# Optimization experiments

Hardware: AMD Instinct MI355X
Metric: run time of the kernel (lower is better)

## Reference

```python
import jax, jax.numpy as jnp
import numpy as np

N = 50000   # nodes
E = 800000  # edges (avg degree 16)
IN = 128    # in_dim
R = 4       # rank
CMB = 64    # combine_dim
H = 4       # heads
D = 64      # hidden_dim per head
NEG_SLOPE = 0.2


def setup_inputs() -> dict:
    key = jax.random.key(0)
    ks = iter(jax.random.split(key, 24))
    def rnd(shape, s):
        return jax.random.normal(next(ks), shape, jnp.float32) * s
    src = jax.random.randint(next(ks), (E,), 0, N, jnp.int32)
    dst = jax.random.randint(next(ks), (E,), 0, N, jnp.int32)
    ones = jnp.ones((N, 1), jnp.float32)
    # buffers built in __init__: features with a trailing ones column
    h_common = jnp.concatenate([rnd((N, IN), 1.0), ones], axis=-1)      # (N, 129)
    h_type = jnp.concatenate([rnd((N, 512), 1.0), ones], axis=-1)       # (N, 513)
    h_rel = jnp.concatenate([rnd((N, 512), 1.0), ones], axis=-1)        # (N, 513)
    return {
        'src': src, 'dst': dst,
        'h_common': h_common, 'h_type': h_type, 'h_rel': h_rel,
        'Wc': rnd((R, IN + 1, CMB), 0.05),
        'Wt': rnd((R, 513, CMB), 0.05),
        'Wr': rnd((R, 513, CMB), 0.05),
        'fw': rnd((1, R), 0.5),
        'fb': rnd((1, CMB), 0.1),
        'W0': rnd((CMB, H * D), 0.05),
        'al0': rnd((H, D), 0.05), 'ar0': rnd((H, D), 0.05),
        'b0': rnd((H * D,), 0.05),
        'W1': rnd((H * D, H * D), 0.05),
        'al1': rnd((H, D), 0.05), 'ar1': rnd((H, D), 0.05),
        'b1': rnd((H * D,), 0.05),
    }


def _gat_layer(h, src, dst, W, al, ar, b, residual):
    # h: (N, F_in) -> out: (N, H*D), attention a: (E, H)
    feat = (h @ W).reshape(N, H, D)
    el = jnp.einsum('nhd,hd->nh', feat, al)  # (N, H)
    er = jnp.einsum('nhd,hd->nh', feat, ar)
    e = jax.nn.leaky_relu(el[src] + er[dst], NEG_SLOPE)  # (E, H)
    # edge softmax over incoming edges of each dst node
    m = jax.ops.segment_max(e, dst, num_segments=N)      # (N, H)
    ee = jnp.exp(e - m[dst])
    s = jax.ops.segment_sum(ee, dst, num_segments=N)
    a = ee / s[dst]                                       # (E, H)
    msg = feat[src] * a[:, :, None]                       # (E, H, D)
    out = jax.ops.segment_sum(msg, dst, num_segments=N)   # (N, H, D)
    if residual:
        out = out + h.reshape(N, H, D)
    out = out + b.reshape(1, H, D)
    return out.reshape(N, H * D), a


def reference(src, dst, h_common, h_type, h_rel, Wc, Wt, Wr, fw, fb,
              W0, al0, ar0, b0, W1, al1, ar1, b1):
    # low-rank trilinear fusion
    fc = jnp.einsum('ni,ric->rnc', h_common, Wc)  # (R, N, CMB)
    ft = jnp.einsum('ni,ric->rnc', h_type, Wt)
    fr = jnp.einsum('ni,ric->rnc', h_rel, Wr)
    zy = fc * ft * fr
    h = jnp.einsum('r,rnc->nc', fw[0], zy) + fb   # (N, CMB)
    h = jax.nn.elu(h)
    # stacked GAT layers
    h, att = _gat_layer(h, src, dst, W0, al0, ar0, b0, residual=False)
    h, att = _gat_layer(h, src, dst, W1, al1, ar1, b1, residual=True)
    return h, att
```

## Files before the change

kernel.cpp:

```cpp
#include <hip/hip_runtime.h>
#include <math.h>

#define NN 50000
#define EE 800000
#define NEG 0.2f
#define NG (NN / 16)

using f32x4  = __attribute__((ext_vector_type(4))) float;
using bf16x8 = __attribute__((ext_vector_type(8))) short;

__device__ __forceinline__ float lrelu(float x){ return x > 0.f ? x : NEG*x; }

__device__ __forceinline__ unsigned short f2b(float f){
    unsigned int u = __float_as_uint(f);
    return (unsigned short)((u + 0x7FFFu + ((u >> 16) & 1u)) >> 16);
}
__device__ __forceinline__ float b2f(unsigned short h){
    return __uint_as_float(((unsigned int)h) << 16);
}

__global__ void pack_w_fusion(const float* __restrict__ W, unsigned short* __restrict__ out,
                              int K, int NKC)
{
    int u = blockIdx.x * blockDim.x + threadIdx.x;
    if (u >= NKC * 16 * 64) return;
    int l = u & 63, chunk = (u >> 6) & 15, kc = u >> 10;
    int ct = chunk >> 2, r = chunk & 3;
    int c = ct * 16 + (l & 15);
    int kb = kc * 32 + (l >> 4) * 8;
    bf16x8 v;
#pragma unroll
    for (int j = 0; j < 8; ++j)
        v[j] = (short)f2b(W[((size_t)r * K + kb + j) * 64 + c]);
    *(bf16x8*)(out + (size_t)u * 8) = v;
}

template<int PERM>
__global__ void pack_w_gemm(const float* __restrict__ W, unsigned short* __restrict__ out,
                            int K, int C)
{
    int NCH = C / 16;
    int total = (K / 32) * NCH * 64;
    int u = blockIdx.x * blockDim.x + threadIdx.x;
    if (u >= total) return;
    int l = u & 63, ch = (u >> 6) % NCH, kc = u / (64 * NCH);
    int c = ch * 16 + (l & 15);
    int kb = kc * 32 + (l >> 4) * 8;
    bf16x8 v;
#pragma unroll
    for (int j = 0; j < 8; ++j) {
        int k = kb + j;
        int ko = PERM ? ((k & 3) * 64 + (k >> 2)) : k;
        v[j] = (short)f2b(W[(size_t)ko * C + c]);
    }
    *(bf16x8*)(out + (size_t)u * 8) = v;
}

template<int KT, int NKC>
__global__ __launch_bounds__(256) void pack_a_tile(
    const float* __restrict__ F, unsigned short* __restrict__ out)
{
    constexpr int TILES = NKC / 4;
    __shared__ float sf[16][130];
    const int tid = threadIdx.x;
    const int g = blockIdx.x / TILES, t = blockIdx.x % TILES;
    const int nb = g * 16, k0 = t * 128;

#pragma unroll
    for (int i = 0; i < 8; ++i) {
        int idx = tid + i * 256;
        int row = idx >> 7, k = idx & 127;
        sf[row][k] = F[(size_t)(nb + row) * KT + k0 + k];
    }
    __syncthreads();
    {
        int kcl = tid >> 6, l = tid & 63;
        int row = l & 15, kb = kcl * 32 + (l >> 4) * 8;
        bf16x8 o;
#pragma unroll
        for (int j = 0; j < 8; ++j) o[j] = (short)f2b(sf[row][kb + j]);
        *(bf16x8*)(out + ((size_t)(g * NKC + t * 4 + kcl) * 64 + l) * 8) = o;
    }
}

template<int K, int NKC>
__device__ __forceinline__ void fusion_pass_rank(
    const unsigned short* __restrict__ ap, const unsigned short* __restrict__ wp,
    const float* __restrict__ W, int G, int w, int l, f32x4 (&acc)[4])
{
    const int c_lo = l & 15;
#pragma unroll
    for (int ct = 0; ct < 4; ++ct) {
        float wi = W[((size_t)w * K + (K - 1)) * 64 + ct * 16 + c_lo];
        acc[ct] = f32x4{wi, wi, wi, wi};
    }
    const unsigned short* ab = ap + (size_t)G * NKC * 512 + l * 8;
    constexpr int D = (NKC < 8) ? NKC : 8;
#pragma unroll
    for (int h = 0; h < NKC / D; ++h) {
        bf16x8 afs[D];
#pragma unroll
        for (int j = 0; j < D; ++j)
            afs[j] = *(const bf16x8*)(ab + (h * D + j) * 512);
        bf16x8 bcur[4];
        {
            const unsigned short* wk = wp + (size_t)(h * D) * 8192 + w * 512 + l * 8;
#pragma unroll
            for (int i = 0; i < 4; ++i) bcur[i] = *(const bf16x8*)(wk + i * 2048);
        }
#pragma unroll
        for (int j = 0; j < D; ++j) {
            bf16x8 bnxt[4];
            if (j + 1 < D) {
                const unsigned short* wk = wp + (size_t)(h * D + j + 1) * 8192 + w * 512 + l * 8;
#pragma unroll
                for (int i = 0; i < 4; ++i) bnxt[i] = *(const bf16x8*)(wk + i * 2048);
            }
#pragma unroll
            for (int i = 0; i < 4; ++i)
                acc[i] = __builtin_amdgcn_mfma_f32_16x16x32_bf16(afs[j], bcur[i], acc[i], 0, 0, 0);
            if (j + 1 < D) {
#pragma unroll
                for (int i = 0; i < 4; ++i) bcur[i] = bnxt[i];
            }
        }
    }
}

__global__ __launch_bounds__(256) void fusion_mfma(
    const unsigned short* __restrict__ apc, const unsigned short* __restrict__ apt,
    const unsigned short* __restrict__ apr,
    const unsigned short* __restrict__ wpc, const unsigned short* __restrict__ wpt,
    const unsigned short* __restrict__ wpr,
    const float* __restrict__ Wc, const float* __restrict__ Wt, const float* __restrict__ Wr,
    const float* __restrict__ fw, const float* __restrict__ fb,
    unsigned short* __restrict__ h0b)
{
    __shared__ float lds[4096];
    const int w = threadIdx.x >> 6, l = threadIdx.x & 63;
    const int G = blockIdx.x;

    f32x4 prod[4], acc[4];
    fusion_pass_rank<129, 4>(apc, wpc, Wc, G, w, l, acc);
#pragma unroll
    for (int ct = 0; ct < 4; ++ct) prod[ct] = acc[ct];
    fusion_pass_rank<513, 16>(apt, wpt, Wt, G, w, l, acc);
#pragma unroll
    for (int ct = 0; ct < 4; ++ct) prod[ct] *= acc[ct];
    fusion_pass_rank<513, 16>(apr, wpr, Wr, G, w, l, acc);
    const float fww = fw[w];
#pragma unroll
    for (int ct = 0; ct < 4; ++ct) {
        prod[ct] = prod[ct] * acc[ct] * fww;
        *(f32x4*)&lds[((w * 4 + ct) * 64 + l) * 4] = prod[ct];
    }
    __syncthreads();

    f32x4 s = *(const f32x4*)&lds[((0 * 4 + w) * 64 + l) * 4];
#pragma unroll
    for (int r = 1; r < 4; ++r)
        s += *(const f32x4*)&lds[((r * 4 + w) * 64 + l) * 4];

    const int c = w * 16 + (l & 15);
    const float fbc = fb[c];
#pragma unroll
    for (int q = 0; q < 4; ++q) {
        int n = G * 16 + (l >> 4) * 4 + q;
        float v = s[q] + fbc;
        v = v > 0.f ? v : expm1f(v);
        h0b[(size_t)n * 64 + c] = f2b(v);
    }
}

template<int K>
__global__ __launch_bounds__(256) void gemm_reg(
    const unsigned short* __restrict__ Ab, const unsigned short* __restrict__ wp,
    unsigned short* __restrict__ featb)
{
    constexpr int NKC = K / 32;
    const int w = threadIdx.x >> 6, l = threadIdx.x & 63;
    const int nb = blockIdx.x * 16;

    f32x4 acc[4];
#pragma unroll
    for (int i = 0; i < 4; ++i) acc[i] = f32x4{0.f, 0.f, 0.f, 0.f};

    const unsigned short* abase = Ab + (size_t)(nb + (l & 15)) * K + (l >> 4) * 8;
    bf16x8 afs[NKC];
#pragma unroll
    for (int kc = 0; kc < NKC; ++kc)
        afs[kc] = *(const bf16x8*)(abase + kc * 32);

    bf16x8 bcur[4];
    {
        const unsigned short* wk = wp + (size_t)(0 * 16 + w * 4) * 512 + l * 8;
#pragma unroll
        for (int i = 0; i < 4; ++i) bcur[i] = *(const bf16x8*)(wk + i * 512);
    }
#pragma unroll
    for (int kc = 0; kc < NKC; ++kc) {
        bf16x8 bnxt[4];
        if (kc + 1 < NKC) {
            const unsigned short* wk = wp + ((size_t)(kc + 1) * 16 + w * 4) * 512 + l * 8;
#pragma unroll
            for (int i = 0; i < 4; ++i) bnxt[i] = *(const bf16x8*)(wk + i * 512);
        }
#pragma unroll
        for (int i = 0; i < 4; ++i)
            acc[i] = __builtin_amdgcn_mfma_f32_16x16x32_bf16(afs[kc], bcur[i], acc[i], 0, 0, 0);
        if (kc + 1 < NKC) {
#pragma unroll
            for (int i = 0; i < 4; ++i) bcur[i] = bnxt[i];
        }
    }
#pragma unroll
    for (int i = 0; i < 4; ++i) {
        int c = (w * 4 + i) * 16 + (l & 15);
        int dm = (c & 63) * 4 + (c >> 6);
#pragma unroll
        for (int q = 0; q < 4; ++q) {
            int n = nb + (l >> 4) * 4 + q;
            featb[(size_t)n * 256 + dm] = f2b(acc[i][q]);
        }
    }
}

__global__ __launch_bounds__(256) void elr_kernel(
    const unsigned short* __restrict__ featb,
    const float* __restrict__ al, const float* __restrict__ ar,
    float* __restrict__ el, float* __restrict__ er)
{
    int wid = (int)((blockIdx.x * (size_t)blockDim.x + threadIdx.x) >> 6);
    int lane = threadIdx.x & 63;
    if (wid >= NN) return;
    ushort4 f4 = *(const ushort4*)(featb + (size_t)wid * 256 + lane * 4);
    float x0 = b2f(f4.x), x1 = b2f(f4.y), x2 = b2f(f4.z), x3 = b2f(f4.w);
    float elh[4], erh[4];
    elh[0] = x0 * al[lane];        erh[0] = x0 * ar[lane];
    elh[1] = x1 * al[64 + lane];   erh[1] = x1 * ar[64 + lane];
    elh[2] = x2 * al[128 + lane];  erh[2] = x2 * ar[128 + lane];
    elh[3] = x3 * al[192 + lane];  erh[3] = x3 * ar[192 + lane];
#pragma unroll
    for (int off = 32; off; off >>= 1) {
#pragma unroll
        for (int h = 0; h < 4; ++h) {
            elh[h] += __shfl_xor(elh[h], off);
            erh[h] += __shfl_xor(erh[h], off);
        }
    }
    if (lane == 0) {
        *(float4*)(el + (size_t)wid * 4) = make_float4(elh[0], elh[1], elh[2], elh[3]);
        *(float4*)(er + (size_t)wid * 4) = make_float4(erh[0], erh[1], erh[2], erh[3]);
    }
}

__global__ void hist_kernel(const int* __restrict__ dst, int* __restrict__ cnt)
{
    int e = blockIdx.x * blockDim.x + threadIdx.x;
    if (e < EE) atomicAdd(&cnt[dst[e]], 1);
}

__global__ __launch_bounds__(1024) void scan_kernel(const int* __restrict__ cnt, int* __restrict__ offs)
{
    __shared__ int tmp[1024];
    const int t = threadIdx.x;
    const int C = (NN + 1023) / 1024;
    int lo = t * C, hi = min(lo + C, NN);
    int s = 0;
    for (int i = lo; i < hi; ++i) s += cnt[i];
    tmp[t] = s;
    __syncthreads();
    for (int off = 1; off < 1024; off <<= 1) {
        int v = (t >= off) ? tmp[t - off] : 0;
        __syncthreads();
        tmp[t] += v;
        __syncthreads();
    }
    int run = (t == 0) ? 0 : tmp[t - 1];
    for (int i = lo; i < hi; ++i) { offs[i] = run; run += cnt[i]; }
    if (t == 1023) offs[NN] = tmp[1023];
}

__global__ void scatter_kernel(const int* __restrict__ dst, const int* __restrict__ offs,
                               int* __restrict__ cur, int* __restrict__ esort)
{
    int e = blockIdx.x * blockDim.x + threadIdx.x;
    if (e < EE) {
        int d = dst[e];
        int p = offs[d] + atomicAdd(&cur[d], 1);
        esort[p] = e;
    }
}

__global__ void edge_prep(const int* __restrict__ esort, const int* __restrict__ src,
                          const int* __restrict__ dst,
                          const float* __restrict__ el, const float* __restrict__ er,
                          float4* __restrict__ eesort, int* __restrict__ srcsort)
{
    int p = blockIdx.x * blockDim.x + threadIdx.x;
    if (p >= EE) return;
    int e = esort[p];
    int s = src[e], d = dst[e];
    srcsort[p] = s;
    float4 l4 = *(const float4*)(el + (size_t)s * 4);
    float4 r4 = *(const float4*)(er + (size_t)d * 4);
    eesort[p] = make_float4(lrelu(l4.x + r4.x), lrelu(l4.y + r4.y),
                            lrelu(l4.z + r4.z), lrelu(l4.w + r4.w));
}

template <int RESID, int WMZ, int WB16, int WF32>
__global__ __launch_bounds__(256) void gat_agg(
    const int* __restrict__ srcsort, const int* __restrict__ offs,
    const unsigned short* __restrict__ featb, float4* __restrict__ eesort,
    const unsigned short* __restrict__ residb, const float* __restrict__ bias,
    float* __restrict__ out, unsigned short* __restrict__ outb,
    float4* __restrict__ mbuf, float4* __restrict__ zbuf)
{
    int n = (int)((blockIdx.x * (size_t)blockDim.x + threadIdx.x) >> 6);
    int lane = threadIdx.x & 63;
    if (n >= NN) return;
    int s0 = offs[n], s1 = offs[n + 1];

    float m0 = -1e30f, m1 = -1e30f, m2 = -1e30f, m3 = -1e30f;
    for (int p = s0 + lane; p < s1; p += 64) {
        float4 v = eesort[p];
        m0 = fmaxf(m0, v.x); m1 = fmaxf(m1, v.y);
        m2 = fmaxf(m2, v.z); m3 = fmaxf(m3, v.w);
    }
#pragma unroll
    for (int off = 32; off; off >>= 1) {
        m0 = fmaxf(m0, __shfl_xor(m0, off));
        m1 = fmaxf(m1, __shfl_xor(m1, off));
        m2 = fmaxf(m2, __shfl_xor(m2, off));
        m3 = fmaxf(m3, __shfl_xor(m3, off));
    }

    float z0 = 0.f, z1 = 0.f, z2 = 0.f, z3 = 0.f;
    for (int p = s0 + lane; p < s1; p += 64) {
        float4 v = eesort[p];
        v.x = expf(v.x - m0); v.y = expf(v.y - m1);
        v.z = expf(v.z - m2); v.w = expf(v.w - m3);
        eesort[p] = v;
        z0 += v.x; z1 += v.y; z2 += v.z; z3 += v.w;
    }
    __threadfence_block();
#pragma unroll
    for (int off = 32; off; off >>= 1) {
        z0 += __shfl_xor(z0, off);
        z1 += __shfl_xor(z1, off);
        z2 += __shfl_xor(z2, off);
        z3 += __shfl_xor(z3, off);
    }
    float i0 = z0 > 0.f ? 1.f / z0 : 0.f;
    float i1 = z1 > 0.f ? 1.f / z1 : 0.f;
    float i2 = z2 > 0.f ? 1.f / z2 : 0.f;
    float i3 = z3 > 0.f ? 1.f / z3 : 0.f;
    if (WMZ && lane == 0) {
        mbuf[n] = make_float4(m0, m1, m2, m3);
        zbuf[n] = make_float4(i0, i1, i2, i3);
    }

    float a0 = 0.f, a1 = 0.f, a2 = 0.f, a3 = 0.f;
    float c0 = 0.f, c1 = 0.f, c2 = 0.f, c3 = 0.f;
    int p = s0;
    for (; p + 3 < s1; p += 4) {
        float4 wA = eesort[p],     wB = eesort[p + 1];
        float4 wC = eesort[p + 2], wD = eesort[p + 3];
        int sA = srcsort[p],     sB = srcsort[p + 1];
        int sC = srcsort[p + 2], sD = srcsort[p + 3];
        ushort4 fA = *(const ushort4*)(featb + (size_t)sA * 256 + lane * 4);
        ushort4 fB = *(const ushort4*)(featb + (size_t)sB * 256 + lane * 4);
        ushort4 fC = *(const ushort4*)(featb + (size_t)sC * 256 + lane * 4);
        ushort4 fD = *(const ushort4*)(featb + (size_t)sD * 256 + lane * 4);
        a0 += wA.x * b2f(fA.x);  c0 += wB.x * b2f(fB.x);
        a1 += wA.y * b2f(fA.y);  c1 += wB.y * b2f(fB.y);
        a2 += wA.z * b2f(fA.z);  c2 += wB.z * b2f(fB.z);
        a3 += wA.w * b2f(fA.w);  c3 += wB.w * b2f(fB.w);
        a0 += wC.x * b2f(fC.x);  c0 += wD.x * b2f(fD.x);
        a1 += wC.y * b2f(fC.y);  c1 += wD.y * b2f(fD.y);
        a2 += wC.z * b2f(fC.z);  c2 += wD.z * b2f(fD.z);
        a3 += wC.w * b2f(fC.w);  c3 += wD.w * b2f(fD.w);
    }
    for (; p < s1; ++p) {
        float4 wA = eesort[p];
        int sA = srcsort[p];
        ushort4 fA = *(const ushort4*)(featb + (size_t)sA * 256 + lane * 4);
        a0 += wA.x * b2f(fA.x);
        a1 += wA.y * b2f(fA.y);
        a2 += wA.z * b2f(fA.z);
        a3 += wA.w * b2f(fA.w);
    }
    a0 += c0; a1 += c1; a2 += c2; a3 += c3;

    float o0 = a0 * i0 + bias[lane];
    float o1 = a1 * i1 + bias[64 + lane];
    float o2 = a2 * i2 + bias[128 + lane];
    float o3 = a3 * i3 + bias[192 + lane];
    if (RESID) {
        ushort4 rp = *(const ushort4*)(residb + (size_t)n * 256 + lane * 4);
        o0 += b2f(rp.x); o1 += b2f(rp.y); o2 += b2f(rp.z); o3 += b2f(rp.w);
    }
    if (WF32) {
        float* op = out + (size_t)n * 256;
        op[lane] = o0;
        op[64 + lane] = o1;
        op[128 + lane] = o2;
        op[192 + lane] = o3;
    }
    if (WB16) {
        ushort4 ob;
        ob.x = f2b(o0); ob.y = f2b(o1); ob.z = f2b(o2); ob.w = f2b(o3);
        *(ushort4*)(outb + (size_t)n * 256 + lane * 4) = ob;
    }
}

__global__ void att_final(const int* __restrict__ src, const int* __restrict__ dst,
                          const float* __restrict__ el, const float* __restrict__ er,
                          const float4* __restrict__ mbuf, const float4* __restrict__ zbuf,
                          float4* __restrict__ att)
{
    int e = blockIdx.x * blockDim.x + threadIdx.x;
    if (e >= EE) return;
    int s = src[e], d = dst[e];
    float4 l4 = *(const float4*)(el + (size_t)s * 4);
    float4 r4 = *(const float4*)(er + (size_t)d * 4);
    float4 m4 = mbuf[d], zi = zbuf[d];
    att[e] = make_float4(expf(lrelu(l4.x + r4.x) - m4.x) * zi.x,
                         expf(lrelu(l4.y + r4.y) - m4.y) * zi.y,
                         expf(lrelu(l4.z + r4.z) - m4.z) * zi.z,
                         expf(lrelu(l4.w + r4.w) - m4.w) * zi.w);
}

extern "C" void kernel_launch(void* const* d_in, const int* in_sizes, int n_in,
                              void* d_out, int out_size, void* d_ws, size_t ws_size,
                              hipStream_t stream)
{
    const int*   src = (const int*)d_in[0];
    const int*   dst = (const int*)d_in[1];
    const float* hc  = (const float*)d_in[2];
    const float* ht  = (const float*)d_in[3];
    const float* hr  = (const float*)d_in[4];
    const float* Wc  = (const float*)d_in[5];
    const float* Wt  = (const float*)d_in[6];
    const float* Wr  = (const float*)d_in[7];
    const float* fw  = (const float*)d_in[8];
    const float* fb  = (const float*)d_in[9];
    const float* W0  = (const float*)d_in[10];
    const float* al0 = (const float*)d_in[11];
    const float* ar0 = (const float*)d_in[12];
    const float* b0  = (const float*)d_in[13];
    const float* W1  = (const float*)d_in[14];
    const float* al1 = (const float*)d_in[15];
    const float* ar1 = (const float*)d_in[16];
    const float* b1  = (const float*)d_in[17];

    char* ws = (char*)d_ws;
    unsigned short* h0b   = (unsigned short*)(ws);
    unsigned short* h1b   = (unsigned short*)(ws + 6400000);
    unsigned short* featb = (unsigned short*)(ws + 32000000);
    float* el    = (float*)(ws + 57600000);
    float* er    = (float*)(ws + 58400000);
    int*   cnt   = (int*)  (ws + 59200000);
    int*   offs  = (int*)  (ws + 59400000);
    int*   esort = (int*)  (ws + 59600128);
    unsigned short* wpc = (unsigned short*)(ws + 62800128);
    unsigned short* wpt = (unsigned short*)(ws + 62865664);
    unsigned short* wpr = (unsigned short*)(ws + 63127808);
    unsigned short* wp0 = (unsigned short*)(ws + 63389952);
    unsigned short* wp1 = (unsigned short*)(ws + 63422720);
    float4* mbuf = (float4*)(ws + 63553792);
    float4* zbuf = (float4*)(ws + 64353792);
    int* srcsort = (int*)  (ws + 65153792);
    if (ws_size < 68353792ull) return;

    float* outh = (float*)d_out;
    float4* atto = (float4*)(outh + (size_t)NN * 256);

    unsigned short* apt = (unsigned short*)d_out;
    unsigned short* apc = (unsigned short*)((char*)d_out + 51200000);
    unsigned short* apr = (unsigned short*)(ws + 6400000);

    pack_w_fusion<<<(4 * 16 * 64 + 255) / 256, 256, 0, stream>>>(Wc, wpc, 129, 4);
    pack_w_fusion<<<(16 * 16 * 64 + 255) / 256, 256, 0, stream>>>(Wt, wpt, 513, 16);
    pack_w_fusion<<<(16 * 16 * 64 + 255) / 256, 256, 0, stream>>>(Wr, wpr, 513, 16);
    pack_w_gemm<0><<<(2 * 16 * 64 + 255) / 256, 256, 0, stream>>>(W0, wp0, 64, 256);
    pack_w_gemm<1><<<(8 * 16 * 64 + 255) / 256, 256, 0, stream>>>(W1, wp1, 256, 256);

    pack_a_tile<129, 4><<<NG * 1, 256, 0, stream>>>(hc, apc);
    pack_a_tile<513, 16><<<NG * 4, 256, 0, stream>>>(ht, apt);
    pack_a_tile<513, 16><<<NG * 4, 256, 0, stream>>>(hr, apr);

    fusion_mfma<<<NG, 256, 0, stream>>>(apc, apt, apr, wpc, wpt, wpr,
                                        Wc, Wt, Wr, fw, fb, h0b);

    hipMemsetAsync(cnt, 0, NN * sizeof(int), stream);
    hist_kernel<<<(EE + 255) / 256, 256, 0, stream>>>(dst, cnt);
    scan_kernel<<<1, 1024, 0, stream>>>(cnt, offs);
    hipMemsetAsync(cnt, 0, NN * sizeof(int), stream);
    scatter_kernel<<<(EE + 255) / 256, 256, 0, stream>>>(dst, offs, cnt, esort);

    gemm_reg<64><<<NG, 256, 0, stream>>>(h0b, wp0, featb);
    elr_kernel<<<(NN * 64 + 255) / 256, 256, 0, stream>>>(featb, al0, ar0, el, er);
    edge_prep<<<(EE + 255) / 256, 256, 0, stream>>>(esort, src, dst, el, er, atto, srcsort);
    gat_agg<0, 0, 1, 0><<<(NN * 64 + 255) / 256, 256, 0, stream>>>(
        srcsort, offs, featb, atto, nullptr, b0, nullptr, h1b, nullptr, nullptr);

    gemm_reg<256><<<NG, 256, 0, stream>>>(h1b, wp1, featb);
    elr_kernel<<<(NN * 64 + 255) / 256, 256, 0, stream>>>(featb, al1, ar1, el, er);
    edge_prep<<<(EE + 255) / 256, 256, 0, stream>>>(esort, src, dst, el, er, atto, srcsort);
    gat_agg<1, 1, 0, 1><<<(NN * 64 + 255) / 256, 256, 0, stream>>>(
        srcsort, offs, featb, atto, h1b, b1, outh, nullptr, mbuf, zbuf);
    att_final<<<(EE + 255) / 256, 256, 0, stream>>>(src, dst, el, er, mbuf, zbuf, atto);
}
```

Before: 628.8 us.

## Split fusion GEMM K-dimension across two wave groups with LDS reduction

The fusion kernel now runs 512 threads per block. Each rank is handled by two waves that each process half of the K chunks for the common, type and relation projections, and the partial sums are combined through LDS before the trilinear product and the rank reduction. This doubles the waves per 16-row tile to expose more memory-level parallelism and shorten the per-wave serial MFMA chain. In exchange it adds several block barriers, twice the LDS, and drops the explicit software prefetch of weight fragments.

Measured after the change: 637.4 us. Within noise of the previous version (+1.4%).

```diff
diff --git a/kernel.cpp b/kernel.cpp
--- a/kernel.cpp
+++ b/kernel.cpp
@@ -84,50 +84,36 @@
 }
 
 template<int K, int NKC>
-__device__ __forceinline__ void fusion_pass_rank(
+__device__ __forceinline__ void fusion_pass_half(
     const unsigned short* __restrict__ ap, const unsigned short* __restrict__ wp,
-    const float* __restrict__ W, int G, int w, int l, f32x4 (&acc)[4])
-{
+    const float* __restrict__ W, int G, int r, int kh, int l, f32x4 (&acc)[4])
+{
+    constexpr int H = NKC / 2;
     const int c_lo = l & 15;
 #pragma unroll
     for (int ct = 0; ct < 4; ++ct) {
-        float wi = W[((size_t)w * K + (K - 1)) * 64 + ct * 16 + c_lo];
-        acc[ct] = f32x4{wi, wi, wi, wi};
-    }
-    const unsigned short* ab = ap + (size_t)G * NKC * 512 + l * 8;
-    constexpr int D = (NKC < 8) ? NKC : 8;
-#pragma unroll
-    for (int h = 0; h < NKC / D; ++h) {
-        bf16x8 afs[D];
-#pragma unroll
-        for (int j = 0; j < D; ++j)
-            afs[j] = *(const bf16x8*)(ab + (h * D + j) * 512);
-        bf16x8 bcur[4];
-        {
-            const unsigned short* wk = wp + (size_t)(h * D) * 8192 + w * 512 + l * 8;
-#pragma unroll
-            for (int i = 0; i < 4; ++i) bcur[i] = *(const bf16x8*)(wk + i * 2048);
-        }
-#pragma unroll
-        for (int j = 0; j < D; ++j) {
-            bf16x8 bnxt[4];
-            if (j + 1 < D) {
-                const unsigned short* wk = wp + (size_t)(h * D + j + 1) * 8192 + w * 512 + l * 8;
-#pragma unroll
-                for (int i = 0; i < 4; ++i) bnxt[i] = *(const bf16x8*)(wk + i * 2048);
-            }
-#pragma unroll
-            for (int i = 0; i < 4; ++i)
-                acc[i] = __builtin_amdgcn_mfma_f32_16x16x32_bf16(afs[j], bcur[i], acc[i], 0, 0, 0);
-            if (j + 1 < D) {
-#pragma unroll
-                for (int i = 0; i < 4; ++i) bcur[i] = bnxt[i];
-            }
-        }
-    }
-}
-
-__global__ __launch_bounds__(256) void fusion_mfma(
+        if (kh == 0) {
+            float wi = W[((size_t)r * K + (K - 1)) * 64 + ct * 16 + c_lo];
+            acc[ct] = f32x4{wi, wi, wi, wi};
+        } else {
+            acc[ct] = f32x4{0.f, 0.f, 0.f, 0.f};
+        }
+    }
+    const unsigned short* ab = ap + (size_t)G * NKC * 512 + (size_t)kh * H * 512 + l * 8;
+    const unsigned short* wb = wp + (size_t)kh * H * 8192 + r * 512 + l * 8;
+#pragma unroll
+    for (int kc = 0; kc < H; ++kc) {
+        bf16x8 af = *(const bf16x8*)(ab + kc * 512);
+        const unsigned short* wk = wb + (size_t)kc * 8192;
+#pragma unroll
+        for (int ct = 0; ct < 4; ++ct) {
+            bf16x8 bf = *(const bf16x8*)(wk + ct * 2048);
+            acc[ct] = __builtin_amdgcn_mfma_f32_16x16x32_bf16(af, bf, acc[ct], 0, 0, 0);
+        }
+    }
+}
+
+__global__ __launch_bounds__(512) void fusion_mfma(
     const unsigned short* __restrict__ apc, const unsigned short* __restrict__ apt,
     const unsigned short* __restrict__ apr,
     const unsigned short* __restrict__ wpc, const unsigned short* __restrict__ wpt,
@@ -136,39 +122,69 @@
     const float* __restrict__ fw, const float* __restrict__ fb,
     unsigned short* __restrict__ h0b)
 {
-    __shared__ float lds[4096];
-    const int w = threadIdx.x >> 6, l = threadIdx.x & 63;
+    __shared__ float lds[8192];
+    const int tid = threadIdx.x;
+    const int w = tid >> 6, l = tid & 63;
+    const int r = w & 3, kh = w >> 2;
     const int G = blockIdx.x;
 
-    f32x4 prod[4], acc[4];
-    fusion_pass_rank<129, 4>(apc, wpc, Wc, G, w, l, acc);
-#pragma unroll
-    for (int ct = 0; ct < 4; ++ct) prod[ct] = acc[ct];
-    fusion_pass_rank<513, 16>(apt, wpt, Wt, G, w, l, acc);
-#pragma unroll
-    for (int ct = 0; ct < 4; ++ct) prod[ct] *= acc[ct];
-    fusion_pass_rank<513, 16>(apr, wpr, Wr, G, w, l, acc);
-    const float fww = fw[w];
-#pragma unroll
-    for (int ct = 0; ct < 4; ++ct) {
-        prod[ct] = prod[ct] * acc[ct] * fww;
-        *(f32x4*)&lds[((w * 4 + ct) * 64 + l) * 4] = prod[ct];
-    }
-    __syncthreads();
-
-    f32x4 s = *(const f32x4*)&lds[((0 * 4 + w) * 64 + l) * 4];
-#pragma unroll
-    for (int r = 1; r < 4; ++r)
-        s += *(const f32x4*)&lds[((r * 4 + w) * 64 + l) * 4];
-
-    const int c = w * 16 + (l & 15);
-    const float fbc = fb[c];
-#pragma unroll
-    for (int q = 0; q < 4; ++q) {
-        int n = G * 16 + (l >> 4) * 4 + q;
-        float v = s[q] + fbc;
-        v = v > 0.f ? v : expm1f(v);
-        h0b[(size_t)n * 64 + c] = f2b(v);
+    f32x4 pC[4], pT[4], pR[4];
+    fusion_pass_half<129, 4>(apc, wpc, Wc, G, r, kh, l, pC);
+    fusion_pass_half<513, 16>(apt, wpt, Wt, G, r, kh, l, pT);
+    fusion_pass_half<513, 16>(apr, wpr, Wr, G, r, kh, l, pR);
+
+    f32x4 fC[4], fT[4], fR[4];
+#pragma unroll
+    for (int ct = 0; ct < 4; ++ct)
+        *(f32x4*)&lds[((w * 4 + ct) * 64 + l) * 4] = pC[ct];
+    __syncthreads();
+    if (kh == 0)
+#pragma unroll
+        for (int ct = 0; ct < 4; ++ct)
+            fC[ct] = pC[ct] + *(const f32x4*)&lds[(((w + 4) * 4 + ct) * 64 + l) * 4];
+    __syncthreads();
+#pragma unroll
+    for (int ct = 0; ct < 4; ++ct)
+        *(f32x4*)&lds[((w * 4 + ct) * 64 + l) * 4] = pT[ct];
+    __syncthreads();
+    if (kh == 0)
+#pragma unroll
+        for (int ct = 0; ct < 4; ++ct)
+            fT[ct] = pT[ct] + *(const f32x4*)&lds[(((w + 4) * 4 + ct) * 64 + l) * 4];
+    __syncthreads();
+#pragma unroll
+    for (int ct = 0; ct < 4; ++ct)
+        *(f32x4*)&lds[((w * 4 + ct) * 64 + l) * 4] = pR[ct];
+    __syncthreads();
+    if (kh == 0)
+#pragma unroll
+        for (int ct = 0; ct < 4; ++ct)
+            fR[ct] = pR[ct] + *(const f32x4*)&lds[(((w + 4) * 4 + ct) * 64 + l) * 4];
+    __syncthreads();
+
+    if (kh == 0) {
+        const float fwr = fw[r];
+#pragma unroll
+        for (int ct = 0; ct < 4; ++ct) {
+            f32x4 prod = fC[ct] * fT[ct] * fR[ct] * fwr;
+            *(f32x4*)&lds[((r * 4 + ct) * 64 + l) * 4] = prod;
+        }
+    }
+    __syncthreads();
+    if (w < 4) {
+        f32x4 s = *(const f32x4*)&lds[((0 * 4 + w) * 64 + l) * 4];
+#pragma unroll
+        for (int rr = 1; rr < 4; ++rr)
+            s += *(const f32x4*)&lds[((rr * 4 + w) * 64 + l) * 4];
+        const int c = w * 16 + (l & 15);
+        const float fbc = fb[c];
+#pragma unroll
+        for (int q = 0; q < 4; ++q) {
+            int n = G * 16 + (l >> 4) * 4 + q;
+            float v = s[q] + fbc;
+            v = v > 0.f ? v : expm1f(v);
+            h0b[(size_t)n * 64 + c] = f2b(v);
+        }
     }
 }
 
@@ -490,7 +506,7 @@
     pack_a_tile<513, 16><<<NG * 4, 256, 0, stream>>>(ht, apt);
     pack_a_tile<513, 16><<<NG * 4, 256, 0, stream>>>(hr, apr);
 
-    fusion_mfma<<<NG, 256, 0, stream>>>(apc, apt, apr, wpc, wpt, wpr,
+    fusion_mfma<<<NG, 512, 0, stream>>>(apc, apt, apr, wpc, wpt, wpr,
                                         Wc, Wt, Wr, fw, fb, h0b);
 
     hipMemsetAsync(cnt, 0, NN * sizeof(int), stream);
```
